# Performance work log

Measured on AMD Instinct MI355X. Metric: run time of the kernel, lower is better.

## Reference

```python
import jax, jax.numpy as jnp
import numpy as np

K = 11      # kernel_size
PAD = 5     # (dilation*(K-1)+1 - 1)//2 with dilation=1


def _unfold(x, k, pad):
    # torch nn.Unfold ordering: channel slowest, then (ki, kj) fastest.
    B, C, H, W = x.shape
    xp = jnp.pad(x, ((0, 0), (0, 0), (pad, pad), (pad, pad)))
    # [B, C, k*k, H, W] -- small fixed loop over the 121 kernel offsets
    cols = jnp.stack([xp[:, :, i:i + H, j:j + W]
                      for i in range(k) for j in range(k)], axis=2)
    return cols.reshape(B, C * k * k, H * W)  # [B, 363, L]


def setup_inputs() -> dict:
    key = jax.random.key(0)
    ks = jax.random.split(key, 4)
    x = jax.random.normal(ks[0], (1, 3, 400, 400), dtype=jnp.float32)
    W1 = jax.random.normal(ks[1], (363, 128), dtype=jnp.float32) * 0.05
    b1 = jnp.zeros((128,), dtype=jnp.float32)
    W2 = jax.random.normal(ks[2], (128, 64), dtype=jnp.float32) * 0.08
    b2 = jnp.zeros((64,), dtype=jnp.float32)
    W3 = jax.random.normal(ks[3], (64, 8), dtype=jnp.float32) * 0.1
    b3 = jnp.zeros((8,), dtype=jnp.float32)
    return {"x": x, "W1": W1, "b1": b1, "W2": W2, "b2": b2, "W3": W3, "b3": b3}


def reference(x, W1, b1, W2, b2, W3, b3):
    B, C, H, W = x.shape
    cols = _unfold(x, K, PAD)                 # [B, 363, H*W]
    h = cols.transpose(0, 2, 1)               # [B, L, 363]
    h = jax.nn.leaky_relu(h @ W1 + b1)        # [B, L, 128], slope 0.01 = torch default
    h = jax.nn.leaky_relu(h @ W2 + b2)        # [B, L, 64]
    h = h @ W3 + b3                           # [B, L, 8]
    # Fold(kernel=1) is a reshape; squeeze(0) + permute -> [H, W, E]
    y = h[0].reshape(H, W, -1)
    # F.normalize(p=2, dim=-1, eps=1e-12)
    n = jnp.maximum(jnp.linalg.norm(y, axis=-1, keepdims=True), 1e-12)
    return y / n
```

## Files before the change

kernel.cpp:

```cpp
#include <hip/hip_runtime.h>
#include <hip/hip_bf16.h>
#include <math.h>

typedef _Float16 f16x8 __attribute__((ext_vector_type(8)));
typedef _Float16 f16x4 __attribute__((ext_vector_type(4)));
typedef float    f32x4 __attribute__((ext_vector_type(4)));

#define IMG   400
#define NPIX  160000
#define NKT1  18
#define W1P   (NKT1*8*64*8)
#define W2P   (4*4*64*8)
#define W3P   (2*64*8)
#define HSS   40
#define XPH   1938

__device__ __forceinline__ void async_cp16(const _Float16* g, _Float16* l) {
    __builtin_amdgcn_global_load_lds(
        (const __attribute__((address_space(1))) uint32_t*)g,
        (__attribute__((address_space(3))) uint32_t*)l, 16, 0, 0);
}

__global__ void pack_weights(const float* __restrict__ W1,
                             const float* __restrict__ W2,
                             const float* __restrict__ W3,
                             _Float16* __restrict__ ws)
{
    int i = blockIdx.x * blockDim.x + threadIdx.x;
    if (i < 576 * 128) {
        int kp = i >> 7, n = i & 127;
        int kt = kp >> 5, kl = kp & 31, q = kl >> 3, j = kl & 7;
        int pair = kp >> 4, kj = kp & 15;
        int c = pair / 12, ki = pair % 12;
        int mt = n >> 4, n15 = n & 15;
        int lane = q * 16 + n15;
        float v = (ki < 11 && kj < 11) ? W1[(c * 121 + ki * 11 + kj) * 128 + n] : 0.0f;
        ws[((kt * 8 + mt) * 64 + lane) * 8 + j] = (_Float16)v;
    } else if (i < 576 * 128 + 128 * 64) {
        int e = i - 576 * 128;
        int kp = e >> 6, n = e & 63;
        int kt = kp >> 5, kl = kp & 31, q = kl >> 3, j = kl & 7;
        int mt = n >> 4, n15 = n & 15;
        int lane = q * 16 + n15;
        ws[W1P + ((kt * 4 + mt) * 64 + lane) * 8 + j] = (_Float16)W2[kp * 64 + n];
    } else if (i < 576 * 128 + 128 * 64 + 64 * 16) {
        int e = i - 576 * 128 - 128 * 64;
        int kp = e >> 4, n = e & 15;
        int kt = kp >> 5, kl = kp & 31, q = kl >> 3, j = kl & 7;
        int lane = q * 16 + n;
        float v = (n < 8) ? W3[kp * 8 + n] : 0.0f;
        ws[W1P + W2P + (kt * 64 + lane) * 8 + j] = (_Float16)v;
    }
}

__global__ __launch_bounds__(256, 4) void fused_unfold_mlp(
    const float* __restrict__ x,
    const float* __restrict__ b1,
    const float* __restrict__ b2,
    const float* __restrict__ b3,
    const _Float16* __restrict__ wpack,
    float* __restrict__ out)
{
    __shared__ __align__(16) _Float16 xs[2 * XPH];
    __shared__ __align__(16) _Float16 w1s[2 * 4096];
    __shared__ __align__(16) _Float16 hs[4][32 * HSS];

    const int tid  = threadIdx.x;
    const int wave = tid >> 6;
    const int lane = tid & 63;
    const int q    = lane >> 4;
    const int n15  = lane & 15;
    const int bx   = blockIdx.x;
    const int by   = blockIdx.y;

    const _Float16* w1p = wpack;
    const _Float16* w2p = wpack + W1P;
    const _Float16* w3p = wpack + W1P + W2P;

    const int kt0 = (bx + by * 25) % NKT1;

    {
        int seg = wave * 2;
        async_cp16(w1p + kt0 * 4096 + seg * 512 + lane * 8, &w1s[seg * 512]);
        async_cp16(w1p + kt0 * 4096 + (seg + 1) * 512 + lane * 8, &w1s[(seg + 1) * 512]);
    }

    for (int w = tid; w < 3 * 19 * 35; w += 256) {
        int col = w % 35;
        int rc  = w / 35;
        int row = rc % 19, c = rc / 19;
        int gy = by * 8 + row - 5;
        int gx = bx * 16 + col - 6;
        float v = 0.0f;
        if ((unsigned)gy < (unsigned)IMG && (unsigned)gx < (unsigned)IMG)
            v = x[c * NPIX + gy * IMG + gx];
        _Float16 hv = (_Float16)v;
        int base = (c * 19 + row) * 34;
        if (col >= 1)  xs[base + col - 1] = hv;
        if (col <= 33) xs[XPH + base + col] = hv;
    }
    __syncthreads();

    const uint32_t* xsd = (const uint32_t*)xs;
    const int h = q >> 1;
    const int u = n15 + (n15 & 1) + ((q & 1) << 3);
    const int bdw0 = (n15 & 1) * (XPH / 2) + (u >> 1);
    int bdwt[2];
#pragma unroll
    for (int t = 0; t < 2; ++t)
        bdwt[t] = bdw0 + (wave * 2 + t + h) * 17;

    f32x4 acc1[2][8];
#pragma unroll
    for (int t = 0; t < 2; ++t)
#pragma unroll
        for (int mt = 0; mt < 8; ++mt)
            acc1[t][mt] = (f32x4){0.f, 0.f, 0.f, 0.f};

    int kt = kt0;
    for (int kk = 0; kk < NKT1; ++kk) {
        if (kk) __syncthreads();
        const int buf  = kk & 1;
        const int nbuf = buf ^ 1;
        const int ktn  = (kt + 1 == NKT1) ? 0 : kt + 1;
        if (kk < NKT1 - 1) {
            int seg = wave * 2;
            async_cp16(w1p + ktn * 4096 + seg * 512 + lane * 8,
                       &w1s[nbuf * 4096 + seg * 512]);
            async_cp16(w1p + ktn * 4096 + (seg + 1) * 512 + lane * 8,
                       &w1s[nbuf * 4096 + (seg + 1) * 512]);
        } else {
            int seg = wave * 2;
#pragma unroll
            for (int s2 = 0; s2 < 2; ++s2)
                async_cp16(w2p + (seg + s2) * 512 + lane * 8,
                           &w1s[(seg + s2) * 512]);
        }

        const int d6  = (kt >= 12) ? 2 : (kt >= 6 ? 1 : 0);
        const int m6  = kt - d6 * 6;
        const int rim = (d6 * 19 + 2 * m6) * 17;

        f16x8 bf[2];
#pragma unroll
        for (int t = 0; t < 2; ++t) {
            union { uint32_t u[4]; f16x8 f; } cv;
#pragma unroll
            for (int m = 0; m < 4; ++m)
                cv.u[m] = xsd[bdwt[t] + rim + m];
            bf[t] = cv.f;
        }
        const _Float16* wb = &w1s[buf * 4096];
#pragma unroll
        for (int mt = 0; mt < 8; ++mt) {
            f16x8 af = *(const f16x8*)(wb + (mt * 64 + lane) * 8);
            acc1[0][mt] = __builtin_amdgcn_mfma_f32_16x16x32_f16(af, bf[0], acc1[0][mt], 0, 0, 0);
            acc1[1][mt] = __builtin_amdgcn_mfma_f32_16x16x32_f16(af, bf[1], acc1[1][mt], 0, 0, 0);
        }
        kt = ktn;
    }
    __syncthreads();

    {
        int seg = wave * 2;
#pragma unroll
        for (int s2 = 0; s2 < 2; ++s2)
            async_cp16(w2p + 4096 + (seg + s2) * 512 + lane * 8,
                       &w1s[4096 + (seg + s2) * 512]);
    }
    __syncthreads();

    const _Float16* w2s = w1s;
    _Float16* hw = hs[wave];

    f32x4 acc2[2][4];
#pragma unroll
    for (int t = 0; t < 2; ++t)
#pragma unroll
        for (int mt = 0; mt < 4; ++mt)
            acc2[t][mt] = (f32x4){0.f, 0.f, 0.f, 0.f};

#pragma unroll
    for (int k2 = 0; k2 < 4; ++k2) {
#pragma unroll
        for (int lm = 0; lm < 2; ++lm) {
            int mt = 2 * k2 + lm;
            float4 bb = *(const float4*)(b1 + mt * 16 + q * 4);
#pragma unroll
            for (int t = 0; t < 2; ++t) {
                f16x4 hv;
#pragma unroll
                for (int r = 0; r < 4; ++r) {
                    float v = acc1[t][mt][r] + ((const float*)&bb)[r];
                    v = fmaxf(v, 0.01f * v);
                    hv[r] = (_Float16)v;
                }
                *(f16x4*)(hw + (t * 16 + n15) * HSS + lm * 16 + q * 4) = hv;
            }
        }
        f16x8 bf[2];
#pragma unroll
        for (int t = 0; t < 2; ++t)
            bf[t] = *(const f16x8*)(hw + (t * 16 + n15) * HSS + q * 8);
#pragma unroll
        for (int mt2 = 0; mt2 < 4; ++mt2) {
            f16x8 af = *(const f16x8*)(w2s + ((k2 * 4 + mt2) * 64 + lane) * 8);
            acc2[0][mt2] = __builtin_amdgcn_mfma_f32_16x16x32_f16(af, bf[0], acc2[0][mt2], 0, 0, 0);
            acc2[1][mt2] = __builtin_amdgcn_mfma_f32_16x16x32_f16(af, bf[1], acc2[1][mt2], 0, 0, 0);
        }
    }

    f16x8 af3[2];
#pragma unroll
    for (int k3 = 0; k3 < 2; ++k3)
        af3[k3] = *(const f16x8*)(w3p + (k3 * 64 + lane) * 8);

    f32x4 acc3[2];
    acc3[0] = (f32x4){0.f, 0.f, 0.f, 0.f};
    acc3[1] = (f32x4){0.f, 0.f, 0.f, 0.f};
#pragma unroll
    for (int k3 = 0; k3 < 2; ++k3) {
#pragma unroll
        for (int lm = 0; lm < 2; ++lm) {
            int mt2 = 2 * k3 + lm;
            float4 bb = *(const float4*)(b2 + mt2 * 16 + q * 4);
#pragma unroll
            for (int t = 0; t < 2; ++t) {
                f16x4 hv;
#pragma unroll
                for (int r = 0; r < 4; ++r) {
                    float v = acc2[t][mt2][r] + ((const float*)&bb)[r];
                    v = fmaxf(v, 0.01f * v);
                    hv[r] = (_Float16)v;
                }
                *(f16x4*)(hw + (t * 16 + n15) * HSS + lm * 16 + q * 4) = hv;
            }
        }
#pragma unroll
        for (int t = 0; t < 2; ++t) {
            f16x8 bf = *(const f16x8*)(hw + (t * 16 + n15) * HSS + q * 8);
            acc3[t] = __builtin_amdgcn_mfma_f32_16x16x32_f16(af3[k3], bf, acc3[t], 0, 0, 0);
        }
    }

    float4 bb3 = make_float4(0.f, 0.f, 0.f, 0.f);
    if (q < 2) bb3 = *(const float4*)(b3 + q * 4);
#pragma unroll
    for (int t = 0; t < 2; ++t) {
        float v0 = acc3[t][0] + bb3.x;
        float v1 = acc3[t][1] + bb3.y;
        float v2 = acc3[t][2] + bb3.z;
        float v3 = acc3[t][3] + bb3.w;
        float s = v0 * v0 + v1 * v1 + v2 * v2 + v3 * v3;
        s += __shfl_xor(s, 16);
        s += __shfl_xor(s, 32);
        float inv = 1.0f / fmaxf(sqrtf(s), 1e-12f);
        if (q < 2) {
            int p = (by * 8 + wave * 2 + t) * IMG + bx * 16 + n15;
            float4 o = make_float4(v0 * inv, v1 * inv, v2 * inv, v3 * inv);
            *(float4*)(out + p * 8 + q * 4) = o;
        }
    }
}

extern "C" void kernel_launch(void* const* d_in, const int* in_sizes, int n_in,
                              void* d_out, int out_size, void* d_ws, size_t ws_size,
                              hipStream_t stream) {
    const float* x  = (const float*)d_in[0];
    const float* W1 = (const float*)d_in[1];
    const float* b1 = (const float*)d_in[2];
    const float* W2 = (const float*)d_in[3];
    const float* b2 = (const float*)d_in[4];
    const float* W3 = (const float*)d_in[5];
    const float* b3 = (const float*)d_in[6];
    float* out = (float*)d_out;
    _Float16* ws = (_Float16*)d_ws;

    pack_weights<<<dim3(324), dim3(256), 0, stream>>>(W1, W2, W3, ws);
    fused_unfold_mlp<<<dim3(25, 50), dim3(256), 0, stream>>>(x, b1, b2, b3, ws, out);
}
```

Measured before the change: 97.79 us.

## Halve block to two waves with four pixel rows each, read W2 from global

The fused kernel now runs 128 threads per block, so each wave covers four output rows instead of two. Each W1 fragment loaded from shared memory therefore feeds four MFMAs rather than two. The W2 staging through shared memory, with its two extra barriers, is removed, and W2 fragments are read directly from global memory. In exchange, accumulator register pressure doubles (acc1 grows to 4x8 f32x4), and each block has half as many threads for the halo load and weight prefetch, which may reduce occupancy.

```diff
diff --git a/kernel.cpp b/kernel.cpp
--- a/kernel.cpp
+++ b/kernel.cpp
@@ -53,7 +53,7 @@
     }
 }
 
-__global__ __launch_bounds__(256, 4) void fused_unfold_mlp(
+__global__ __launch_bounds__(128, 2) void fused_unfold_mlp(
     const float* __restrict__ x,
     const float* __restrict__ b1,
     const float* __restrict__ b2,
@@ -63,7 +63,7 @@
 {
     __shared__ __align__(16) _Float16 xs[2 * XPH];
     __shared__ __align__(16) _Float16 w1s[2 * 4096];
-    __shared__ __align__(16) _Float16 hs[4][32 * HSS];
+    __shared__ __align__(16) _Float16 hs[2][64 * HSS];
 
     const int tid  = threadIdx.x;
     const int wave = tid >> 6;
@@ -80,12 +80,14 @@
     const int kt0 = (bx + by * 25) % NKT1;
 
     {
-        int seg = wave * 2;
-        async_cp16(w1p + kt0 * 4096 + seg * 512 + lane * 8, &w1s[seg * 512]);
-        async_cp16(w1p + kt0 * 4096 + (seg + 1) * 512 + lane * 8, &w1s[(seg + 1) * 512]);
-    }
-
-    for (int w = tid; w < 3 * 19 * 35; w += 256) {
+        int seg = wave * 4;
+#pragma unroll
+        for (int s = 0; s < 4; ++s)
+            async_cp16(w1p + kt0 * 4096 + (seg + s) * 512 + lane * 8,
+                       &w1s[(seg + s) * 512]);
+    }
+
+    for (int w = tid; w < 3 * 19 * 35; w += 128) {
         int col = w % 35;
         int rc  = w / 35;
         int row = rc % 19, c = rc / 19;
@@ -105,14 +107,14 @@
     const int h = q >> 1;
     const int u = n15 + (n15 & 1) + ((q & 1) << 3);
     const int bdw0 = (n15 & 1) * (XPH / 2) + (u >> 1);
-    int bdwt[2];
-#pragma unroll
-    for (int t = 0; t < 2; ++t)
-        bdwt[t] = bdw0 + (wave * 2 + t + h) * 17;
-
-    f32x4 acc1[2][8];
-#pragma unroll
-    for (int t = 0; t < 2; ++t)
+    int bdwt[4];
+#pragma unroll
+    for (int t = 0; t < 4; ++t)
+        bdwt[t] = bdw0 + (wave * 4 + t + h) * 17;
+
+    f32x4 acc1[4][8];
+#pragma unroll
+    for (int t = 0; t < 4; ++t)
 #pragma unroll
         for (int mt = 0; mt < 8; ++mt)
             acc1[t][mt] = (f32x4){0.f, 0.f, 0.f, 0.f};
@@ -124,26 +126,20 @@
         const int nbuf = buf ^ 1;
         const int ktn  = (kt + 1 == NKT1) ? 0 : kt + 1;
         if (kk < NKT1 - 1) {
-            int seg = wave * 2;
-            async_cp16(w1p + ktn * 4096 + seg * 512 + lane * 8,
-                       &w1s[nbuf * 4096 + seg * 512]);
-            async_cp16(w1p + ktn * 4096 + (seg + 1) * 512 + lane * 8,
-                       &w1s[nbuf * 4096 + (seg + 1) * 512]);
-        } else {
-            int seg = wave * 2;
-#pragma unroll
-            for (int s2 = 0; s2 < 2; ++s2)
-                async_cp16(w2p + (seg + s2) * 512 + lane * 8,
-                           &w1s[(seg + s2) * 512]);
+            int seg = wave * 4;
+#pragma unroll
+            for (int s = 0; s < 4; ++s)
+                async_cp16(w1p + ktn * 4096 + (seg + s) * 512 + lane * 8,
+                           &w1s[nbuf * 4096 + (seg + s) * 512]);
         }
 
         const int d6  = (kt >= 12) ? 2 : (kt >= 6 ? 1 : 0);
         const int m6  = kt - d6 * 6;
         const int rim = (d6 * 19 + 2 * m6) * 17;
 
-        f16x8 bf[2];
-#pragma unroll
-        for (int t = 0; t < 2; ++t) {
+        f16x8 bf[4];
+#pragma unroll
+        for (int t = 0; t < 4; ++t) {
             union { uint32_t u[4]; f16x8 f; } cv;
 #pragma unroll
             for (int m = 0; m < 4; ++m)
@@ -154,28 +150,18 @@
 #pragma unroll
         for (int mt = 0; mt < 8; ++mt) {
             f16x8 af = *(const f16x8*)(wb + (mt * 64 + lane) * 8);
-            acc1[0][mt] = __builtin_amdgcn_mfma_f32_16x16x32_f16(af, bf[0], acc1[0][mt], 0, 0, 0);
-            acc1[1][mt] = __builtin_amdgcn_mfma_f32_16x16x32_f16(af, bf[1], acc1[1][mt], 0, 0, 0);
+#pragma unroll
+            for (int t = 0; t < 4; ++t)
+                acc1[t][mt] = __builtin_amdgcn_mfma_f32_16x16x32_f16(af, bf[t], acc1[t][mt], 0, 0, 0);
         }
         kt = ktn;
     }
-    __syncthreads();
-
-    {
-        int seg = wave * 2;
-#pragma unroll
-        for (int s2 = 0; s2 < 2; ++s2)
-            async_cp16(w2p + 4096 + (seg + s2) * 512 + lane * 8,
-                       &w1s[4096 + (seg + s2) * 512]);
-    }
-    __syncthreads();
-
-    const _Float16* w2s = w1s;
+
     _Float16* hw = hs[wave];
 
-    f32x4 acc2[2][4];
-#pragma unroll
-    for (int t = 0; t < 2; ++t)
+    f32x4 acc2[4][4];
+#pragma unroll
+    for (int t = 0; t < 4; ++t)
 #pragma unroll
         for (int mt = 0; mt < 4; ++mt)
             acc2[t][mt] = (f32x4){0.f, 0.f, 0.f, 0.f};
@@ -187,7 +173,7 @@
             int mt = 2 * k2 + lm;
             float4 bb = *(const float4*)(b1 + mt * 16 + q * 4);
 #pragma unroll
-            for (int t = 0; t < 2; ++t) {
+            for (int t = 0; t < 4; ++t) {
                 f16x4 hv;
 #pragma unroll
                 for (int r = 0; r < 4; ++r) {
@@ -198,15 +184,16 @@
                 *(f16x4*)(hw + (t * 16 + n15) * HSS + lm * 16 + q * 4) = hv;
             }
         }
-        f16x8 bf[2];
-#pragma unroll
-        for (int t = 0; t < 2; ++t)
+        f16x8 bf[4];
+#pragma unroll
+        for (int t = 0; t < 4; ++t)
             bf[t] = *(const f16x8*)(hw + (t * 16 + n15) * HSS + q * 8);
 #pragma unroll
         for (int mt2 = 0; mt2 < 4; ++mt2) {
-            f16x8 af = *(const f16x8*)(w2s + ((k2 * 4 + mt2) * 64 + lane) * 8);
-            acc2[0][mt2] = __builtin_amdgcn_mfma_f32_16x16x32_f16(af, bf[0], acc2[0][mt2], 0, 0, 0);
-            acc2[1][mt2] = __builtin_amdgcn_mfma_f32_16x16x32_f16(af, bf[1], acc2[1][mt2], 0, 0, 0);
+            f16x8 af = *(const f16x8*)(w2p + ((k2 * 4 + mt2) * 64 + lane) * 8);
+#pragma unroll
+            for (int t = 0; t < 4; ++t)
+                acc2[t][mt2] = __builtin_amdgcn_mfma_f32_16x16x32_f16(af, bf[t], acc2[t][mt2], 0, 0, 0);
         }
     }
 
@@ -215,9 +202,10 @@
     for (int k3 = 0; k3 < 2; ++k3)
         af3[k3] = *(const f16x8*)(w3p + (k3 * 64 + lane) * 8);
 
-    f32x4 acc3[2];
-    acc3[0] = (f32x4){0.f, 0.f, 0.f, 0.f};
-    acc3[1] = (f32x4){0.f, 0.f, 0.f, 0.f};
+    f32x4 acc3[4];
+#pragma unroll
+    for (int t = 0; t < 4; ++t)
+        acc3[t] = (f32x4){0.f, 0.f, 0.f, 0.f};
 #pragma unroll
     for (int k3 = 0; k3 < 2; ++k3) {
 #pragma unroll
@@ -225,7 +213,7 @@
             int mt2 = 2 * k3 + lm;
             float4 bb = *(const float4*)(b2 + mt2 * 16 + q * 4);
 #pragma unroll
-            for (int t = 0; t < 2; ++t) {
+            for (int t = 0; t < 4; ++t) {
                 f16x4 hv;
 #pragma unroll
                 for (int r = 0; r < 4; ++r) {
@@ -237,7 +225,7 @@
             }
         }
 #pragma unroll
-        for (int t = 0; t < 2; ++t) {
+        for (int t = 0; t < 4; ++t) {
             f16x8 bf = *(const f16x8*)(hw + (t * 16 + n15) * HSS + q * 8);
             acc3[t] = __builtin_amdgcn_mfma_f32_16x16x32_f16(af3[k3], bf, acc3[t], 0, 0, 0);
         }
@@ -246,7 +234,7 @@
     float4 bb3 = make_float4(0.f, 0.f, 0.f, 0.f);
     if (q < 2) bb3 = *(const float4*)(b3 + q * 4);
 #pragma unroll
-    for (int t = 0; t < 2; ++t) {
+    for (int t = 0; t < 4; ++t) {
         float v0 = acc3[t][0] + bb3.x;
         float v1 = acc3[t][1] + bb3.y;
         float v2 = acc3[t][2] + bb3.z;
@@ -256,7 +244,7 @@
         s += __shfl_xor(s, 32);
         float inv = 1.0f / fmaxf(sqrtf(s), 1e-12f);
         if (q < 2) {
-            int p = (by * 8 + wave * 2 + t) * IMG + bx * 16 + n15;
+            int p = (by * 8 + wave * 4 + t) * IMG + bx * 16 + n15;
             float4 o = make_float4(v0 * inv, v1 * inv, v2 * inv, v3 * inv);
             *(float4*)(out + p * 8 + q * 4) = o;
         }
@@ -277,5 +265,5 @@
     _Float16* ws = (_Float16*)d_ws;
 
     pack_weights<<<dim3(324), dim3(256), 0, stream>>>(W1, W2, W3, ws);
-    fused_unfold_mlp<<<dim3(25, 50), dim3(256), 0, stream>>>(x, b1, b2, b3, ws, out);
-}
+    fused_unfold_mlp<<<dim3(25, 50), dim3(128), 0, stream>>>(x, b1, b2, b3, ws, out);
+}
```

New measurement: 109.7 us. 12.1% more time.
